# Kernel tuning notes

Measured on AMD Instinct MI355X. Metric: run time of the kernel, lower is better.

## Reference

```python
import jax, jax.numpy as jnp
import numpy as np

N_NODES = 100000


def _gcn_norm(edge_index, num_nodes):
    # PyG GCNConv default: add self-loops, symmetric deg^{-1/2} normalization.
    src, dst = edge_index[0], edge_index[1]
    loops = jnp.arange(num_nodes, dtype=edge_index.dtype)
    src_f = jnp.concatenate([src, loops])  # [E+N]
    dst_f = jnp.concatenate([dst, loops])
    deg = jax.ops.segment_sum(jnp.ones_like(dst_f, dtype=jnp.float32), dst_f, num_segments=num_nodes)
    dinv = jnp.where(deg > 0, jax.lax.rsqrt(deg), 0.0)
    norm = dinv[src_f] * dinv[dst_f]  # [E+N]
    return src_f, dst_f, norm


def _gcn_conv(h, src_f, dst_f, norm, W, b, num_nodes):
    # linear transform first (reduces gather/scatter width), then normalized scatter-add
    hw = h @ W  # [N, out]
    msgs = hw[src_f] * norm[:, None]  # [E+N, out]
    out = jax.ops.segment_sum(msgs, dst_f, num_segments=num_nodes)
    return out + b


def setup_inputs() -> dict:
    key = jax.random.key(0)
    ks = jax.random.split(key, 8)
    N, E, F, H = N_NODES, 3200000, 512, 256
    x = jax.random.normal(ks[0], (N, F), dtype=jnp.float32)
    edge_index = jax.random.randint(ks[1], (2, E), 0, N, dtype=jnp.int64)
    W1 = jax.random.normal(ks[2], (F, H), dtype=jnp.float32) * (1.0 / np.sqrt(F))
    b1 = jnp.zeros((H,), dtype=jnp.float32)
    Wc = jax.random.normal(ks[3], (H, 40), dtype=jnp.float32) * (1.0 / np.sqrt(H))
    bc = jnp.zeros((40,), dtype=jnp.float32)
    Wk = jax.random.normal(ks[4], (H, 16), dtype=jnp.float32) * (1.0 / np.sqrt(H))
    bk = jnp.zeros((16,), dtype=jnp.float32)
    Wd = jax.random.normal(ks[5], (H, 1), dtype=jnp.float32) * (1.0 / np.sqrt(H))
    bd = jnp.zeros((1,), dtype=jnp.float32)
    return {"x": x, "edge_index": edge_index, "W1": W1, "b1": b1, "Wc": Wc, "bc": bc, "Wk": Wk, "bk": bk, "Wd": Wd, "bd": bd}


def reference(x, edge_index, W1, b1, Wc, bc, Wk, bk, Wd, bd):
    N = N_NODES
    src_f, dst_f, norm = _gcn_norm(edge_index, N)
    h = jax.nn.relu(_gcn_conv(x, src_f, dst_f, norm, W1, b1, N))
    # dropout is identity at inference (training=False)
    main_out = _gcn_conv(h, src_f, dst_f, norm, Wc, bc, N)
    clus_out = _gcn_conv(h, src_f, dst_f, norm, Wk, bk, N)
    deg_out = _gcn_conv(h, src_f, dst_f, norm, Wd, bd, N)
    return (main_out, clus_out, deg_out)
```

## Files before the change

kernel.cpp:

```cpp
#include <hip/hip_runtime.h>

#define NN 100000

typedef __attribute__((ext_vector_type(8))) __bf16 bf16x8;
typedef __attribute__((ext_vector_type(8))) unsigned short ushort8v;
typedef __attribute__((ext_vector_type(4))) float f32x4;

__device__ __forceinline__ float bf2f(unsigned short u) {
    union { unsigned int ui; float f; } c;
    c.ui = ((unsigned int)u) << 16;
    return c.f;
}

__device__ __forceinline__ unsigned short f2bf(float f) {
    union { float ff; unsigned int ui; } c;
    c.ff = f;
    unsigned int u = c.ui;
    u += 0x7FFFu + ((u >> 16) & 1u);
    return (unsigned short)(u >> 16);
}

__device__ __forceinline__ unsigned short trunc_hi(float x, float& resid) {
    union { float f; unsigned int u; } c, h;
    c.f = x;
    h.u = c.u & 0xFFFF0000u;
    resid = x - h.f;
    return (unsigned short)(c.u >> 16);
}

__device__ __forceinline__ unsigned short trunc_bits(float x) {
    union { float f; unsigned int u; } c;
    c.f = x;
    return (unsigned short)(c.u >> 16);
}

__global__ void MultiTaskGCN_37623913513359_kernel() {}

__global__ void probe_fmt(const int* ei, const unsigned short* x, int* flags) {
    if (blockIdx.x != 0 || threadIdx.x != 0) return;
    int any = 0;
    for (int i = 0; i < 64; ++i) any |= ei[2 * i + 1];
    flags[0] = (any == 0) ? 1 : 0;
    int bf = 1;
    for (int i = 0; i < 512; ++i) {
        float v = bf2f(x[2 * i]);
        float av = v < 0.0f ? -v : v;
        if (!(v == v) || av > 1.0e6f) { bf = 0; break; }
    }
    flags[1] = bf;
}

__device__ __forceinline__ int edge_src(const int* ei, int is64, int e) {
    if (is64) return ei[2 * e];
    return ei[e];
}
__device__ __forceinline__ int edge_dst(const int* ei, int is64, int e, int E) {
    if (is64) return ei[2 * (E + e)];
    return ei[E + e];
}

__device__ __forceinline__ float load_f(const void* p, int dt, size_t i) {
    if (dt) return bf2f(((const unsigned short*)p)[i]);
    return ((const float*)p)[i];
}

__global__ __launch_bounds__(256) void count_deg_i(const int* ei, const int* flags,
                                                   int* degi, int E) {
    int t = blockIdx.x * 256 + threadIdx.x;
    if (t >= E) return;
    int is64 = flags[0];
    int s = edge_src(ei, is64, t);
    int d = edge_dst(ei, is64, t, E);
    if (((unsigned)s) >= NN || ((unsigned)d) >= NN) return;
    atomicAdd(&degi[d], 1);
}

__global__ __launch_bounds__(256) void make_dinv(const int* degi, float* dinv) {
    int i = blockIdx.x * 256 + threadIdx.x;
    if (i < NN) dinv[i] = rsqrtf((float)degi[i] + 1.0f);
}

__global__ __launch_bounds__(1024) void scan_rowptr(const int* degi, int* rowptr) {
    __shared__ int part[1024];
    int tid = threadIdx.x;
    const int chunk = (NN + 1023) / 1024;
    int base = tid * chunk;
    int s = 0;
    for (int j = 0; j < chunk; ++j) {
        int i = base + j;
        if (i < NN) s += degi[i];
    }
    part[tid] = s;
    __syncthreads();
    for (int off = 1; off < 1024; off <<= 1) {
        int v = (tid >= off) ? part[tid - off] : 0;
        __syncthreads();
        part[tid] += v;
        __syncthreads();
    }
    int run = (tid == 0) ? 0 : part[tid - 1];
    for (int j = 0; j < chunk; ++j) {
        int i = base + j;
        if (i < NN) {
            rowptr[i] = run;
            run += degi[i];
        }
    }
    if (tid == 1023) rowptr[NN] = part[1023];
}

__global__ __launch_bounds__(256) void fill_csr(const int* ei, const int* flags,
                                                const float* dinv, const int* rowptr,
                                                int* cursor, unsigned long long* csr,
                                                int E) {
    int t = blockIdx.x * 256 + threadIdx.x;
    if (t >= E) return;
    int is64 = flags[0];
    int s = edge_src(ei, is64, t);
    int d = edge_dst(ei, is64, t, E);
    if (((unsigned)s) >= NN || ((unsigned)d) >= NN) return;
    int pos = rowptr[d] + atomicAdd(&cursor[d], 1);
    float w = dinv[s] * dinv[d];
    union { float ff; unsigned int ui; } c;
    c.ff = w;
    csr[pos] = ((unsigned long long)c.ui << 32) | (unsigned int)s;
}

__global__ __launch_bounds__(256) void prep_w1t(const void* W1, const int* flags,
                                                unsigned short* hi, unsigned short* lo) {
    int t = blockIdx.x * 256 + threadIdx.x;
    if (t >= 256 * 512) return;
    int n = t >> 9, k = t & 511;
    float v = load_f(W1, flags[1], (size_t)k * 256 + n);
    float r;
    hi[t] = trunc_hi(v, r);
    lo[t] = trunc_bits(r);
}

__global__ __launch_bounds__(256) void prep_wcat(const void* Wc, const void* Wk,
                                                 const void* Wd, const int* flags,
                                                 unsigned short* hi, unsigned short* lo) {
    int t = blockIdx.x * 256 + threadIdx.x;
    if (t >= 64 * 256) return;
    int n = t >> 8, k = t & 255;
    int dt = flags[1];
    float v = 0.0f;
    if (n < 40) v = load_f(Wc, dt, (size_t)k * 40 + n);
    else if (n < 56) v = load_f(Wk, dt, (size_t)k * 16 + (n - 40));
    else if (n == 56) v = load_f(Wd, dt, k);
    float r;
    hi[t] = trunc_hi(v, r);
    lo[t] = trunc_bits(r);
}


template<int NB>
struct StageRegs {
    ushort8v ah[2], al[2], bh[NB], bl[NB];
};

template<int NB>
__device__ __forceinline__ StageRegs<NB> stage_load(const void* A, const unsigned short* BTh,
                                                    const unsigned short* BTl, int M, int K,
                                                    int m0, int n0, int k0,
                                                    int lane, int wid, int adt, bool blo) {
    StageRegs<NB> s;
#pragma unroll
    for (int half = 0; half < 2; ++half) {
        int gr = m0 + lane + half * 64;
        if (gr >= M) gr = M - 1;
        if (adt == 0) {
            const float* ap = (const float*)A + (size_t)gr * K + k0 + wid * 8;
            f32x4 v0 = *(const f32x4*)ap;
            f32x4 v1 = *(const f32x4*)(ap + 4);
            ushort8v h, l;
#pragma unroll
            for (int j = 0; j < 4; ++j) {
                float r;
                h[j] = trunc_hi(v0[j], r);
                l[j] = trunc_bits(r);
            }
#pragma unroll
            for (int j = 0; j < 4; ++j) {
                float r;
                h[4 + j] = trunc_hi(v1[j], r);
                l[4 + j] = trunc_bits(r);
            }
            s.ah[half] = h;
            s.al[half] = l;
        } else {
            s.ah[half] = *(const ushort8v*)((const unsigned short*)A + (size_t)gr * K + k0 + wid * 8);
        }
    }
#pragma unroll
    for (int nb = 0; nb < NB; ++nb) {
        size_t o = (size_t)(n0 + lane + nb * 64) * K + k0 + wid * 8;
        s.bh[nb] = *(const ushort8v*)(BTh + o);
        if (blo) s.bl[nb] = *(const ushort8v*)(BTl + o);
    }
    return s;
}

template<int BM, int BN, int NB>
__device__ __forceinline__ void stage_write(ushort8v (&As)[2][4][BM], ushort8v (&Bs)[2][4][BN],
                                            const StageRegs<NB>& s, int lane, int wid,
                                            bool alo, bool blo) {
    As[0][wid][lane] = s.ah[0];
    As[0][wid][lane + 64] = s.ah[1];
    if (alo) {
        As[1][wid][lane] = s.al[0];
        As[1][wid][lane + 64] = s.al[1];
    }
#pragma unroll
    for (int nb = 0; nb < NB; ++nb) {
        Bs[0][wid][lane + nb * 64] = s.bh[nb];
        if (blo) Bs[1][wid][lane + nb * 64] = s.bl[nb];
    }
}

template<int BM, int BN, int NF>
__device__ __forceinline__ void mfma_step(const ushort8v (&As)[2][4][BM],
                                          const ushort8v (&Bs)[2][4][BN],
                                          f32x4 (&acc)[4][NF],
                                          int wm, int wn, int lane, bool alo, bool blo) {
    const int lr = lane & 15;
    const int lk = lane >> 4;
    bf16x8 ah[4], al[4];
#pragma unroll
    for (int i = 0; i < 4; ++i) {
        ah[i] = *(const bf16x8*)&As[0][lk][wm * 64 + i * 16 + lr];
        if (alo) al[i] = *(const bf16x8*)&As[1][lk][wm * 64 + i * 16 + lr];
    }
    bf16x8 bh[NF], bl[NF];
#pragma unroll
    for (int j = 0; j < NF; ++j) {
        bh[j] = *(const bf16x8*)&Bs[0][lk][wn * (BN / 2) + j * 16 + lr];
        if (blo) bl[j] = *(const bf16x8*)&Bs[1][lk][wn * (BN / 2) + j * 16 + lr];
    }
#pragma unroll
    for (int i = 0; i < 4; ++i) {
#pragma unroll
        for (int j = 0; j < NF; ++j) {
            acc[i][j] = __builtin_amdgcn_mfma_f32_16x16x32_bf16(ah[i], bh[j], acc[i][j], 0, 0, 0);
            if (blo) acc[i][j] = __builtin_amdgcn_mfma_f32_16x16x32_bf16(ah[i], bl[j], acc[i][j], 0, 0, 0);
            if (alo) acc[i][j] = __builtin_amdgcn_mfma_f32_16x16x32_bf16(al[i], bh[j], acc[i][j], 0, 0, 0);
        }
    }
}

template<int BN, int NF>
__global__ __launch_bounds__(256) void gemm_mfma(const void* A, const unsigned short* BTh,
                                                 const unsigned short* BTl, unsigned short* C,
                                                 int M, int N, int K, const int* flags, int amode) {
    constexpr int BM = 128;
    constexpr int NB = BN / 64;
    __shared__ ushort8v As[2][4][BM];
    __shared__ ushort8v Bs[2][4][BN];

    const int tid = threadIdx.x;
    const int lane = tid & 63;
    const int wid = tid >> 6;
    const int wm = wid >> 1;
    const int wn = wid & 1;
    const int dt = flags[1];
    const int adt = (amode == 0) ? dt : 1;
    const bool alo = (adt == 0);
    const bool blo = (dt == 0);
    const int m0 = blockIdx.x * BM;
    const int n0 = blockIdx.y * BN;

    f32x4 zero = {0.0f, 0.0f, 0.0f, 0.0f};
    f32x4 acc[4][NF];
#pragma unroll
    for (int i = 0; i < 4; ++i)
#pragma unroll
        for (int j = 0; j < NF; ++j) acc[i][j] = zero;

    StageRegs<NB> sA = stage_load<NB>(A, BTh, BTl, M, K, m0, n0, 0, lane, wid, adt, blo);
    const int nT = K >> 5;
    for (int t = 0; t < nT; t += 2) {
        __syncthreads();
        stage_write<BM, BN, NB>(As, Bs, sA, lane, wid, alo, blo);
        __syncthreads();
        StageRegs<NB> sB = stage_load<NB>(A, BTh, BTl, M, K, m0, n0, (t + 1) << 5, lane, wid, adt, blo);
        mfma_step<BM, BN, NF>(As, Bs, acc, wm, wn, lane, alo, blo);
        __syncthreads();
        stage_write<BM, BN, NB>(As, Bs, sB, lane, wid, alo, blo);
        __syncthreads();
        if (t + 2 < nT)
            sA = stage_load<NB>(A, BTh, BTl, M, K, m0, n0, (t + 2) << 5, lane, wid, adt, blo);
        mfma_step<BM, BN, NF>(As, Bs, acc, wm, wn, lane, alo, blo);
    }

    const int lr = lane & 15;
    const int lq = lane >> 4;
#pragma unroll
    for (int i = 0; i < 4; ++i) {
#pragma unroll
        for (int rr = 0; rr < 4; ++rr) {
            int row = m0 + wm * 64 + i * 16 + lq * 4 + rr;
            if (row < M) {
#pragma unroll
                for (int j = 0; j < NF; ++j) {
                    int col = n0 + wn * (BN / 2) + j * 16 + lr;
                    C[(size_t)row * N + col] = f2bf(acc[i][j][rr]);
                }
            }
        }
    }
}

__global__ __launch_bounds__(256) void gather_h(const int* rowptr,
                                                const unsigned long long* csr,
                                                const unsigned short* xwb,
                                                const void* b1,
                                                const float* dinv,
                                                const int* flags,
                                                unsigned short* hb) {
    int node = (blockIdx.x * 256 + threadIdx.x) >> 6;
    int lane = threadIdx.x & 63;
    if (node >= NN) return;
    int beg = rowptr[node], end = rowptr[node + 1];
    const unsigned short* xp = xwb + (size_t)lane * 4;

    float a0[4] = {0.f, 0.f, 0.f, 0.f};
    float a1[4] = {0.f, 0.f, 0.f, 0.f};
    float a2[4] = {0.f, 0.f, 0.f, 0.f};
    float a3[4] = {0.f, 0.f, 0.f, 0.f};

    int e = beg;
    for (; e + 4 <= end; e += 4) {
        unsigned long long p0 = csr[e + 0];
        unsigned long long p1 = csr[e + 1];
        unsigned long long p2 = csr[e + 2];
        unsigned long long p3 = csr[e + 3];
        unsigned long long v0 = *(const unsigned long long*)(xp + ((size_t)(unsigned int)p0) * 256);
        unsigned long long v1 = *(const unsigned long long*)(xp + ((size_t)(unsigned int)p1) * 256);
        unsigned long long v2 = *(const unsigned long long*)(xp + ((size_t)(unsigned int)p2) * 256);
        unsigned long long v3 = *(const unsigned long long*)(xp + ((size_t)(unsigned int)p3) * 256);
        union { unsigned int ui; float ff; } w0, w1, w2, w3;
        w0.ui = (unsigned int)(p0 >> 32);
        w1.ui = (unsigned int)(p1 >> 32);
        w2.ui = (unsigned int)(p2 >> 32);
        w3.ui = (unsigned int)(p3 >> 32);
        a0[0] += w0.ff * bf2f((unsigned short)v0);
        a0[1] += w0.ff * bf2f((unsigned short)(v0 >> 16));
        a0[2] += w0.ff * bf2f((unsigned short)(v0 >> 32));
        a0[3] += w0.ff * bf2f((unsigned short)(v0 >> 48));
        a1[0] += w1.ff * bf2f((unsigned short)v1);
        a1[1] += w1.ff * bf2f((unsigned short)(v1 >> 16));
        a1[2] += w1.ff * bf2f((unsigned short)(v1 >> 32));
        a1[3] += w1.ff * bf2f((unsigned short)(v1 >> 48));
        a2[0] += w2.ff * bf2f((unsigned short)v2);
        a2[1] += w2.ff * bf2f((unsigned short)(v2 >> 16));
        a2[2] += w2.ff * bf2f((unsigned short)(v2 >> 32));
        a2[3] += w2.ff * bf2f((unsigned short)(v2 >> 48));
        a3[0] += w3.ff * bf2f((unsigned short)v3);
        a3[1] += w3.ff * bf2f((unsigned short)(v3 >> 16));
        a3[2] += w3.ff * bf2f((unsigned short)(v3 >> 32));
        a3[3] += w3.ff * bf2f((unsigned short)(v3 >> 48));
    }
    for (; e < end; ++e) {
        unsigned long long p = csr[e];
        union { unsigned int ui; float ff; } c;
        c.ui = (unsigned int)(p >> 32);
        unsigned long long v = *(const unsigned long long*)(xp + ((size_t)(unsigned int)p) * 256);
        a0[0] += c.ff * bf2f((unsigned short)v);
        a0[1] += c.ff * bf2f((unsigned short)(v >> 16));
        a0[2] += c.ff * bf2f((unsigned short)(v >> 32));
        a0[3] += c.ff * bf2f((unsigned short)(v >> 48));
    }

    int dt = flags[1];
    float di = dinv[node];
    float sl = di * di;
    size_t base = (size_t)node * 256 + lane * 4;
    unsigned long long v = *(const unsigned long long*)(xwb + base);
    float r0 = sl * bf2f((unsigned short)v)         + (a0[0] + a1[0]) + (a2[0] + a3[0]) + load_f(b1, dt, lane * 4 + 0);
    float r1 = sl * bf2f((unsigned short)(v >> 16)) + (a0[1] + a1[1]) + (a2[1] + a3[1]) + load_f(b1, dt, lane * 4 + 1);
    float r2 = sl * bf2f((unsigned short)(v >> 32)) + (a0[2] + a1[2]) + (a2[2] + a3[2]) + load_f(b1, dt, lane * 4 + 2);
    float r3 = sl * bf2f((unsigned short)(v >> 48)) + (a0[3] + a1[3]) + (a2[3] + a3[3]) + load_f(b1, dt, lane * 4 + 3);
    if (r0 < 0.f) r0 = 0.f;
    if (r1 < 0.f) r1 = 0.f;
    if (r2 < 0.f) r2 = 0.f;
    if (r3 < 0.f) r3 = 0.f;
    unsigned long long o = (unsigned long long)f2bf(r0)
                         | ((unsigned long long)f2bf(r1) << 16)
                         | ((unsigned long long)f2bf(r2) << 32)
                         | ((unsigned long long)f2bf(r3) << 48);
    *(unsigned long long*)(hb + base) = o;
}

__global__ __launch_bounds__(256) void gather_out(const int* rowptr,
                                                  const unsigned long long* csr,
                                                  const unsigned short* hw2b,
                                                  const void* bc, const void* bk,
                                                  const void* bd,
                                                  const float* dinv,
                                                  const int* flags,
                                                  void* outv) {
    int node = (blockIdx.x * 256 + threadIdx.x) >> 6;
    int lane = threadIdx.x & 63;
    if (node >= NN) return;
    int beg = rowptr[node], end = rowptr[node + 1];
    const unsigned short* hp = hw2b + lane;

    float c0 = 0.f, c1 = 0.f, c2 = 0.f, c3 = 0.f;
    float c4 = 0.f, c5 = 0.f, c6 = 0.f, c7 = 0.f;

    int e = beg;
    for (; e + 8 <= end; e += 8) {
        unsigned long long p0 = csr[e + 0];
        unsigned long long p1 = csr[e + 1];
        unsigned long long p2 = csr[e + 2];
        unsigned long long p3 = csr[e + 3];
        unsigned long long p4 = csr[e + 4];
        unsigned long long p5 = csr[e + 5];
        unsigned long long p6 = csr[e + 6];
        unsigned long long p7 = csr[e + 7];
        float f0 = bf2f(hp[((size_t)(unsigned int)p0) * 64]);
        float f1 = bf2f(hp[((size_t)(unsigned int)p1) * 64]);
        float f2 = bf2f(hp[((size_t)(unsigned int)p2) * 64]);
        float f3 = bf2f(hp[((size_t)(unsigned int)p3) * 64]);
        float f4 = bf2f(hp[((size_t)(unsigned int)p4) * 64]);
        float f5 = bf2f(hp[((size_t)(unsigned int)p5) * 64]);
        float f6 = bf2f(hp[((size_t)(unsigned int)p6) * 64]);
        float f7 = bf2f(hp[((size_t)(unsigned int)p7) * 64]);
        union { unsigned int ui; float ff; } w0, w1, w2, w3, w4, w5, w6, w7;
        w0.ui = (unsigned int)(p0 >> 32);
        w1.ui = (unsigned int)(p1 >> 32);
        w2.ui = (unsigned int)(p2 >> 32);
        w3.ui = (unsigned int)(p3 >> 32);
        w4.ui = (unsigned int)(p4 >> 32);
        w5.ui = (unsigned int)(p5 >> 32);
        w6.ui = (unsigned int)(p6 >> 32);
        w7.ui = (unsigned int)(p7 >> 32);
        c0 += w0.ff * f0;
        c1 += w1.ff * f1;
        c2 += w2.ff * f2;
        c3 += w3.ff * f3;
        c4 += w4.ff * f4;
        c5 += w5.ff * f5;
        c6 += w6.ff * f6;
        c7 += w7.ff * f7;
    }
    for (; e < end; ++e) {
        unsigned long long p = csr[e];
        union { unsigned int ui; float ff; } c;
        c.ui = (unsigned int)(p >> 32);
        c0 += c.ff * bf2f(hp[((size_t)(unsigned int)p) * 64]);
    }
    float acc = ((c0 + c1) + (c2 + c3)) + ((c4 + c5) + (c6 + c7));

    if (lane >= 57) return;
    int dt = flags[1];
    float di = dinv[node];
    float v = di * di * bf2f(hw2b[(size_t)node * 64 + lane]) + acc;
    size_t o;
    if (lane < 40) {
        v += load_f(bc, dt, lane);
        o = (size_t)node * 40 + lane;
    } else if (lane < 56) {
        v += load_f(bk, dt, lane - 40);
        o = (size_t)NN * 40 + (size_t)node * 16 + (lane - 40);
    } else {
        v += load_f(bd, dt, 0);
        o = (size_t)NN * 56 + node;
    }
    if (dt) ((unsigned short*)outv)[o] = f2bf(v);
    else ((float*)outv)[o] = v;
}

extern "C" void kernel_launch(void* const* d_in, const int* in_sizes, int n_in,
                              void* d_out, int out_size, void* d_ws, size_t ws_size,
                              hipStream_t stream) {
    const void* x  = d_in[0];
    const int* ei  = (const int*)d_in[1];
    const void* W1 = d_in[2];
    const void* b1 = d_in[3];
    const void* Wc = d_in[4];
    const void* bc = d_in[5];
    const void* Wk = d_in[6];
    const void* bk = d_in[7];
    const void* Wd = d_in[8];
    const void* bd = d_in[9];

    int E = in_sizes[1] / 2;

    hipError_t herr = hipSuccess;
    hipError_t e;

    char* ws = (char*)d_ws;
    size_t off = 0;
    int* flags = (int*)(ws + off);                      off += 256;
    float* dinv = (float*)(ws + off);                   off += 400128;
    int* rowptr = (int*)(ws + off);                     off += 400384;
    char* scr = ws + off;                               off += 800256;
    int* degi = (int*)scr;
    int* cursor = (int*)(scr + 400128);
    unsigned short* w1t_hi = (unsigned short*)scr;
    unsigned short* w1t_lo = (unsigned short*)(scr + 262144);
    unsigned short* wct_hi = (unsigned short*)(scr + 524288);
    unsigned short* wct_lo = (unsigned short*)(scr + 557056);
    unsigned long long* csr = (unsigned long long*)(ws + off); off += (size_t)E * 8;
    unsigned short* xwb = (unsigned short*)(ws + off);  off += (size_t)NN * 256 * 2;
    unsigned short* hb = (unsigned short*)(ws + off);   off += (size_t)NN * 256 * 2;
    unsigned short* hw2b = (unsigned short*)(ws + off); off += (size_t)NN * 64 * 2;

    int ws_bad = (off > ws_size) ? 1 : 0;

    if (!ws_bad) {
        e = hipMemsetAsync(degi, 0, (size_t)NN * 4, stream);
        if (herr == hipSuccess && e != hipSuccess) herr = e;
        e = hipMemsetAsync(cursor, 0, (size_t)NN * 4, stream);
        if (herr == hipSuccess && e != hipSuccess) herr = e;

        probe_fmt<<<1, 64, 0, stream>>>(ei, (const unsigned short*)x, flags);
        count_deg_i<<<(E + 255) / 256, 256, 0, stream>>>(ei, flags, degi, E);
        make_dinv<<<(NN + 255) / 256, 256, 0, stream>>>(degi, dinv);
        scan_rowptr<<<1, 1024, 0, stream>>>(degi, rowptr);
        fill_csr<<<(E + 255) / 256, 256, 0, stream>>>(ei, flags, dinv, rowptr,
                                                      cursor, csr, E);

        prep_w1t<<<512, 256, 0, stream>>>(W1, flags, w1t_hi, w1t_lo);
        prep_wcat<<<64, 256, 0, stream>>>(Wc, Wk, Wd, flags, wct_hi, wct_lo);

        {
            dim3 grid((NN + 127) / 128, 2);
            gemm_mfma<128, 4><<<grid, 256, 0, stream>>>(x, w1t_hi, w1t_lo, xwb,
                                                        NN, 256, 512, flags, 0);
        }
        gather_h<<<(NN + 3) / 4, 256, 0, stream>>>(rowptr, csr, xwb, b1, dinv,
                                                   flags, hb);

        {
            dim3 grid((NN + 127) / 128, 1);
            gemm_mfma<64, 2><<<grid, 256, 0, stream>>>(hb, wct_hi, wct_lo, hw2b,
                                                       NN, 64, 256, flags, 2);
        }
        gather_out<<<(NN + 3) / 4, 256, 0, stream>>>(rowptr, csr, hw2b, bc, bk, bd,
                                                     dinv, flags, d_out);
    }

    e = hipGetLastError();
    if (herr == hipSuccess && e != hipSuccess) herr = e;

    if (herr != hipSuccess) {
        (void)hipMemsetAsync(d_out, 0x41 + ((int)herr & 7), 128, stream);
    }
    if (ws_bad) {
        (void)hipMemsetAsync(d_out, 0x58, 128, stream);
    }
}
```

Before: 1.346 ms.

## Pre-split x into bf16 hi/lo and stream GEMM tiles via global_load_lds

Adds a split_x pass that converts fp32 x into interleaved bf16 hi/lo pairs once, and a new GEMM kernel that loads A and B tiles straight into LDS with global_load_lds instead of staging them through registers. The new GEMM is used for both the first layer (when workspace allows) and the output-head GEMM. The goal is to take the per-tile fp32-to-bf16 splitting and register staging out of the GEMM inner loop. The cost is an extra full pass that reads x and writes 200MB, and a loop that is not double-buffered and synchronises on every K step.

```diff
diff --git a/kernel.cpp b/kernel.cpp
--- a/kernel.cpp
+++ b/kernel.cpp
@@ -32,6 +32,13 @@
     union { float f; unsigned int u; } c;
     c.f = x;
     return (unsigned short)(c.u >> 16);
+}
+
+__device__ __forceinline__ void gload_lds16(const void* g, void* l) {
+    void* gnc = (void*)g;
+    __builtin_amdgcn_global_load_lds((__attribute__((address_space(1))) void*)gnc,
+                                     (__attribute__((address_space(3))) void*)l,
+                                     16, 0, 0);
 }
 
 __global__ void MultiTaskGCN_37623913513359_kernel() {}
@@ -151,6 +158,152 @@
     float r;
     hi[t] = trunc_hi(v, r);
     lo[t] = trunc_bits(r);
+}
+
+__global__ __launch_bounds__(256) void split_x(const float* x, unsigned char* xs,
+                                               const int* flags, long long ngrp) {
+    if (flags[1]) return;
+    long long i0 = (long long)blockIdx.x * 256 + threadIdx.x;
+    long long stride = (long long)gridDim.x * 256;
+    for (long long g = i0; g < ngrp; g += stride) {
+        const float* p = x + g * 8;
+        f32x4 v0 = *(const f32x4*)p;
+        f32x4 v1 = *(const f32x4*)(p + 4);
+        ushort8v h, l;
+        float r;
+#pragma unroll
+        for (int j = 0; j < 4; ++j) {
+            h[j] = trunc_hi(v0[j], r);
+            l[j] = trunc_bits(r);
+        }
+#pragma unroll
+        for (int j = 0; j < 4; ++j) {
+            h[4 + j] = trunc_hi(v1[j], r);
+            l[4 + j] = trunc_bits(r);
+        }
+        *(ushort8v*)(xs + g * 32) = h;
+        *(ushort8v*)(xs + g * 32 + 16) = l;
+    }
+}
+
+
+template<int BN, int NF>
+__global__ __launch_bounds__(256, 3) void gemm_gl(const void* A, const void* Axs,
+                                                  const unsigned short* BTh,
+                                                  const unsigned short* BTl,
+                                                  unsigned short* C,
+                                                  int M, int N, int K,
+                                                  const int* flags, int amode) {
+    constexpr int BM = 128;
+    constexpr int HB = BN / 64;
+    __shared__ ushort8v smem[4 * BM + 4 * BM + 4 * BN + 4 * BN];
+    ushort8v* Ash = smem;
+    ushort8v* Asl = smem + 4 * BM;
+    ushort8v* Bsh = smem + 8 * BM;
+    ushort8v* Bsl = smem + 8 * BM + 4 * BN;
+
+    const int tid = threadIdx.x;
+    const int lane = tid & 63;
+    const int wid = tid >> 6;
+    const int wm = wid >> 1;
+    const int wn = wid & 1;
+    const int dt = flags[1];
+
+    const unsigned char* Ab;
+    int rowbytes, gstep, alo;
+    if (amode == 0 && dt == 0) {
+        Ab = (const unsigned char*)Axs; rowbytes = K * 4; gstep = 32; alo = 1;
+    } else {
+        Ab = (const unsigned char*)A;   rowbytes = K * 2; gstep = 16; alo = 0;
+    }
+    const int blo = (dt == 0) ? 1 : 0;
+
+    const int m0 = blockIdx.x * BM;
+    const int n0 = blockIdx.y * BN;
+
+    f32x4 zero = {0.0f, 0.0f, 0.0f, 0.0f};
+    f32x4 acc[4][NF];
+#pragma unroll
+    for (int i = 0; i < 4; ++i)
+#pragma unroll
+        for (int j = 0; j < NF; ++j) acc[i][j] = zero;
+
+    const int nT = K >> 5;
+    for (int t = 0; t < nT; ++t) {
+        const int k0 = t << 5;
+        const int G0 = t << 2;
+        for (int q = wid; q < 8; q += 4) {
+            int kg = q >> 1, hf = q & 1;
+            int row = m0 + hf * 64 + lane;
+            if (row >= M) row = M - 1;
+            const unsigned char* g = Ab + (size_t)row * rowbytes + (size_t)(G0 + kg) * gstep;
+            gload_lds16(g, Ash + kg * BM + hf * 64);
+            if (alo) gload_lds16(g + 16, Asl + kg * BM + hf * 64);
+        }
+        for (int q = wid; q < 4 * HB; q += 4) {
+            int kg = q / HB, hf = q % HB;
+            int col = n0 + hf * 64 + lane;
+            const unsigned short* gh = BTh + (size_t)col * K + k0 + kg * 8;
+            gload_lds16(gh, Bsh + kg * BN + hf * 64);
+            if (blo) gload_lds16(BTl + (size_t)col * K + k0 + kg * 8, Bsl + kg * BN + hf * 64);
+        }
+        __syncthreads();
+
+        {
+            const int lr = lane & 15;
+            const int lk = lane >> 4;
+            bf16x8 ah[4], al[4];
+#pragma unroll
+            for (int i = 0; i < 4; ++i) {
+                ah[i] = *(const bf16x8*)&Ash[lk * BM + wm * 64 + i * 16 + lr];
+                if (alo) al[i] = *(const bf16x8*)&Asl[lk * BM + wm * 64 + i * 16 + lr];
+            }
+            bf16x8 bh[NF], bl[NF];
+#pragma unroll
+            for (int j = 0; j < NF; ++j) {
+                bh[j] = *(const bf16x8*)&Bsh[lk * BN + wn * (NF * 16) + j * 16 + lr];
+                if (blo) bl[j] = *(const bf16x8*)&Bsl[lk * BN + wn * (NF * 16) + j * 16 + lr];
+            }
+#pragma unroll
+            for (int i = 0; i < 4; ++i) {
+#pragma unroll
+                for (int j = 0; j < NF; ++j) {
+                    acc[i][j] = __builtin_amdgcn_mfma_f32_16x16x32_bf16(ah[i], bh[j], acc[i][j], 0, 0, 0);
+                    if (blo) acc[i][j] = __builtin_amdgcn_mfma_f32_16x16x32_bf16(ah[i], bl[j], acc[i][j], 0, 0, 0);
+                    if (alo) acc[i][j] = __builtin_amdgcn_mfma_f32_16x16x32_bf16(al[i], bh[j], acc[i][j], 0, 0, 0);
+                }
+            }
+        }
+        __syncthreads();
+    }
+
+    unsigned short* cs = (unsigned short*)smem;
+    const int lr = lane & 15;
+    const int lq = lane >> 4;
+#pragma unroll
+    for (int i = 0; i < 4; ++i) {
+#pragma unroll
+        for (int j = 0; j < NF; ++j) {
+#pragma unroll
+            for (int rr = 0; rr < 4; ++rr) {
+                int row = wm * 64 + i * 16 + lq * 4 + rr;
+                int col = wn * (NF * 16) + j * 16 + lr;
+                cs[row * BN + col] = f2bf(acc[i][j][rr]);
+            }
+        }
+    }
+    __syncthreads();
+    constexpr int TOTAL = BM * BN;
+#pragma unroll
+    for (int base = 0; base < TOTAL; base += 2048) {
+        int idx = base + tid * 8;
+        int r = idx / BN;
+        int c = idx % BN;
+        int grow = m0 + r;
+        if (grow < M) {
+            *(ushort8v*)(C + (size_t)grow * N + n0 + c) = *(const ushort8v*)(cs + idx);
+        }
+    }
 }
 
 
@@ -509,6 +662,10 @@
 
     int ws_bad = (off > ws_size) ? 1 : 0;
 
+    unsigned char* xs = (unsigned char*)(ws + off);
+    size_t xs_bytes = (size_t)NN * 512 * 4;
+    int fast = (!ws_bad && (off + xs_bytes) <= ws_size) ? 1 : 0;
+
     if (!ws_bad) {
         e = hipMemsetAsync(degi, 0, (size_t)NN * 4, stream);
         if (herr == hipSuccess && e != hipSuccess) herr = e;
@@ -525,7 +682,13 @@
         prep_w1t<<<512, 256, 0, stream>>>(W1, flags, w1t_hi, w1t_lo);
         prep_wcat<<<64, 256, 0, stream>>>(Wc, Wk, Wd, flags, wct_hi, wct_lo);
 
-        {
+        if (fast) {
+            split_x<<<4096, 256, 0, stream>>>((const float*)x, xs, flags,
+                                              (long long)NN * 512 / 8);
+            dim3 grid((NN + 127) / 128, 2);
+            gemm_gl<128, 4><<<grid, 256, 0, stream>>>(x, xs, w1t_hi, w1t_lo, xwb,
+                                                      NN, 256, 512, flags, 0);
+        } else {
             dim3 grid((NN + 127) / 128, 2);
             gemm_mfma<128, 4><<<grid, 256, 0, stream>>>(x, w1t_hi, w1t_lo, xwb,
                                                         NN, 256, 512, flags, 0);
@@ -535,8 +698,8 @@
 
         {
             dim3 grid((NN + 127) / 128, 1);
-            gemm_mfma<64, 2><<<grid, 256, 0, stream>>>(hb, wct_hi, wct_lo, hw2b,
-                                                       NN, 64, 256, flags, 2);
+            gemm_gl<64, 2><<<grid, 256, 0, stream>>>(hb, nullptr, wct_hi, wct_lo,
+                                                     hw2b, NN, 64, 256, flags, 2);
         }
         gather_out<<<(NN + 3) / 4, 256, 0, stream>>>(rowptr, csr, hw2b, bc, bk, bd,
                                                      dinv, flags, d_out);
```

New measurement: 1.282 ms. 4.7% less time.
